# Kernel tuning notes

Measured on AMD Instinct MI355X. Metric: run time of the kernel, lower is better.

## Reference

```python
import jax, jax.numpy as jnp
import numpy as np

WS = 7          # window size
DISP = 3        # WS // 2 cyclic shift displacement
HEADS = 3
HD = 32         # head dim
DIM = 96        # hidden dim (= HEADS*HD)
DS = 4          # patch-merging downscale factor
NWH = 16        # windows per spatial dim after merging (112/7)
SCALE = HD ** -0.5


def _rel_indices(ws):
    idx = np.array([[x, y] for x in range(ws) for y in range(ws)])
    return idx[None, :, :] - idx[:, None, :] + ws - 1  # (ws^2, ws^2, 2)


def _shift_mask(ws, disp, nwh, nww):
    n = ws * ws
    ul = np.zeros((n, n), np.float32)
    ul[-disp * ws:, :-disp * ws] = -np.inf
    ul[:-disp * ws, -disp * ws:] = -np.inf
    lr = np.zeros((ws, ws, ws, ws), np.float32)
    lr[:, -disp:, :, :-disp] = -np.inf
    lr[:, :-disp, :, -disp:] = -np.inf
    lr = lr.reshape(n, n)
    m = np.zeros((nwh * nww, n, n), np.float32)
    m[-nww:] += ul            # last row of windows: upper/lower mask
    m[nww - 1::nww] += lr     # last column of windows: left/right mask
    return m

REL = jnp.asarray(_rel_indices(WS))                       # (49,49,2) int
SHIFT_MASK = jnp.asarray(_shift_mask(WS, DISP, NWH, NWH))  # (256,49,49)


def _layernorm(x, g, b):
    mu = jnp.mean(x, axis=-1, keepdims=True)
    var = jnp.var(x, axis=-1, keepdims=True)
    return (x - mu) * jax.lax.rsqrt(var + 1e-5) * g + b


def _window_attention(y, wqkv, pos_tab, wo, bo, shifted):
    # y: (b, nh, nw, DIM)
    if shifted:
        y = jnp.roll(y, (-DISP, -DISP), axis=(1, 2))
    b, nh, nw, _ = y.shape
    nwh, nww = nh // WS, nw // WS
    qkv = y @ wqkv  # (b, nh, nw, 3*DIM); last dim layout [q|k|v]
    qkv = qkv.reshape(b, nwh, WS, nww, WS, 3, HEADS, HD)
    qkv = qkv.transpose(5, 0, 6, 1, 3, 2, 4, 7).reshape(3, b, HEADS, nwh * nww, WS * WS, HD)
    q, k, v = qkv[0], qkv[1], qkv[2]
    dots = jnp.einsum('bhwid,bhwjd->bhwij', q, k) * SCALE  # (b,h,nwin,49,49)
    dots = dots + pos_tab[REL[..., 0], REL[..., 1]]        # relative pos bias
    if shifted:
        dots = dots + SHIFT_MASK[None, None]
    attn = jax.nn.softmax(dots, axis=-1)
    o = jnp.einsum('bhwij,bhwjd->bhwid', attn, v)
    o = o.reshape(b, HEADS, nwh, nww, WS, WS, HD)
    o = o.transpose(0, 2, 4, 3, 5, 1, 6).reshape(b, nh, nw, HEADS * HD)
    o = o @ wo + bo
    if shifted:
        o = jnp.roll(o, (DISP, DISP), axis=(1, 2))
    return o


def setup_inputs() -> dict:
    key = jax.random.key(0)
    ks = jax.random.split(key, 8)
    B, C, H, W = 16, 3, 448, 448
    s = 0.02
    return {
        'x': jax.random.normal(ks[0], (B, C, H, W), jnp.float32),
        'pm_w': jax.random.normal(ks[1], (C * DS * DS, DIM), jnp.float32) * s,
        'pm_b': jnp.zeros((DIM,), jnp.float32),
        'ln1_g': jnp.ones((2, DIM), jnp.float32),
        'ln1_b': jnp.zeros((2, DIM), jnp.float32),
        'qkv_w': jax.random.normal(ks[2], (2, DIM, 3 * HEADS * HD), jnp.float32) * s,
        'pos': jax.random.normal(ks[3], (2, 2 * WS - 1, 2 * WS - 1), jnp.float32),
        'out_w': jax.random.normal(ks[4], (2, HEADS * HD, DIM), jnp.float32) * s,
        'out_b': jnp.zeros((2, DIM), jnp.float32),
        'ln2_g': jnp.ones((2, DIM), jnp.float32),
        'ln2_b': jnp.zeros((2, DIM), jnp.float32),
        'ff1_w': jax.random.normal(ks[5], (2, DIM, 4 * DIM), jnp.float32) * s,
        'ff1_b': jnp.zeros((2, 4 * DIM), jnp.float32),
        'ff2_w': jax.random.normal(ks[6], (2, 4 * DIM, DIM), jnp.float32) * s,
        'ff2_b': jnp.zeros((2, DIM), jnp.float32),
    }


def reference(x, pm_w, pm_b, ln1_g, ln1_b, qkv_w, pos, out_w, out_b,
              ln2_g, ln2_b, ff1_w, ff1_b, ff2_w, ff2_b):
    b, c, h, w = x.shape
    # PatchMerging: Unfold(k=s=DS) orders channels as (c, kh, kw)
    xp = x.reshape(b, c, h // DS, DS, w // DS, DS)
    xp = xp.transpose(0, 2, 4, 1, 3, 5).reshape(b, h // DS, w // DS, c * DS * DS)
    xp = xp @ pm_w + pm_b  # (b, 112, 112, DIM)
    for i, shifted in enumerate((False, True)):
        y = _layernorm(xp, ln1_g[i], ln1_b[i])
        xp = xp + _window_attention(y, qkv_w[i], pos[i], out_w[i], out_b[i], shifted)
        y = _layernorm(xp, ln2_g[i], ln2_b[i])
        y = jax.nn.gelu(y @ ff1_w[i] + ff1_b[i], approximate=False) @ ff2_w[i] + ff2_b[i]
        xp = xp + y
    return xp.transpose(0, 3, 1, 2)  # (b, DIM, 112, 112)
```

## Files before the change

### kernel.cpp

```cpp
#include <hip/hip_runtime.h>
#include <hip/hip_bf16.h>

#define HW 112
#define NPIX (HW*HW)
#define NTOK_TOTAL (16*NPIX)
#define SCALE_ATTN 0.17677669529663689f

typedef short bf16x8 __attribute__((ext_vector_type(8)));
typedef float f32x4 __attribute__((ext_vector_type(4)));

__device__ __forceinline__ short f2bf(float f) {
    __hip_bfloat16 h = __float2bfloat16(f);
    return *reinterpret_cast<short*>(&h);
}

__device__ __forceinline__ float gelu_tanh(float x) {
    float t  = x * x;
    float m1 = fmaf(0.071354816f, t, 1.5957691f);
    float e  = __expf(x * m1);
    float r  = __builtin_amdgcn_rcpf(e + 1.0f);
    return fmaf(-x, r, x);
}

__device__ __forceinline__ void gload_lds16(const short* g, short* l) {
    __builtin_amdgcn_global_load_lds(
        (__attribute__((address_space(1))) void*)g,
        (__attribute__((address_space(3))) void*)l,
        16, 0, 0);
}

__global__ __launch_bounds__(256) void patch_merge_kernel(
    const float* __restrict__ x, const float* __restrict__ pm_w,
    const float* __restrict__ pm_b, float* __restrict__ xp)
{
    __shared__ float w_lds[48*96];
    __shared__ float in_lds[16*52];
    __shared__ float b_lds[96];
    const int t = threadIdx.x;
    const int jt = blockIdx.x, i = blockIdx.y, b = blockIdx.z;
    const int j0 = jt * 16;

    for (int e = t; e < 48*96; e += 256) w_lds[e] = pm_w[e];
    if (t < 96) b_lds[t] = pm_b[t];
    for (int e = t; e < 768; e += 256) {
        int r = e >> 6, col = e & 63;
        int c = r >> 2, kh = r & 3;
        float v = x[(((size_t)(b*3 + c))*448 + (4*i + kh))*448 + 4*j0 + col];
        in_lds[(col >> 2)*52 + c*16 + kh*4 + (col & 3)] = v;
    }
    __syncthreads();
    for (int e = t; e < 16*96; e += 256) {
        int pos = e / 96, ch = e % 96;
        float acc = b_lds[ch];
        #pragma unroll
        for (int k = 0; k < 48; ++k)
            acc = fmaf(in_lds[pos*52 + k], w_lds[k*96 + ch], acc);
        xp[((size_t)((b*HW + i)*HW) + j0 + pos)*96 + ch] = acc;
    }
}

__global__ __launch_bounds__(256) void prep_weights_kernel(
    const float* __restrict__ ff1, const float* __restrict__ ff2,
    const float* __restrict__ qkv_w, const float* __restrict__ out_w,
    const float* __restrict__ pos,
    short* __restrict__ wF, short* __restrict__ qkvT,
    short* __restrict__ outT, float* __restrict__ pos49)
{
    int i = blockIdx.x * 256 + threadIdx.x;
    if (i < 147456) {
        int l = i / 73728, r = i % 73728;
        int c = r / 18432, r2 = r % 18432;
        int half = r2 / 9216, r3 = r2 % 9216;
        int f = r3 / 512, L = (r3 % 512) / 8, j = r3 % 8;
        int ks = f / 6, n = f % 6;
        float val;
        if (half == 0) {
            int k  = ks*32 + (L >> 4)*8 + j;
            int ng = c*96 + n*16 + (L & 15);
            val = ff1[(size_t)l*36864 + (size_t)k*384 + ng];
        } else {
            int kg = c*96 + ks*32 + (L >> 4)*8 + j;
            int ng = n*16 + (L & 15);
            val = ff2[(size_t)l*36864 + (size_t)kg*96 + ng];
        }
        wF[i] = f2bf(val);
    } else if (i < 202752) {
        int j = i - 147456;
        int l = j / 27648, r = j % 27648, n = r / 96, k = r % 96;
        float v = qkv_w[(size_t)l*27648 + k*288 + n];
        if (n < 96) v *= SCALE_ATTN;
        qkvT[j] = f2bf(v);
    } else if (i < 221184) {
        int j = i - 202752;
        int l = j / 9216, r = j % 9216, n = r / 96, k = r % 96;
        outT[j] = f2bf(out_w[(size_t)l*9216 + k*96 + n]);
    } else if (i < 226280) {
        int j = i - 221184;
        int l = j / 2548, r = j % 2548, ti = r / 52, tj = r % 52;
        float v = 0.f;
        if (ti < 49 && tj < 49) {
            int xi = ti / 7, yi = ti % 7, xj = tj / 7, yj = tj % 7;
            v = pos[l*169 + (xj - xi + 6)*13 + (yj - yi + 6)];
        }
        pos49[j] = v;
    }
}

template<bool SHIFTED>
__global__ __launch_bounds__(192, 4) void attn_mfma_kernel(
    float* __restrict__ xp,
    const float* __restrict__ ln_g, const float* __restrict__ ln_b,
    const short* __restrict__ qkvT,
    const float* __restrict__ pos49,
    const short* __restrict__ outT,
    const float* __restrict__ out_b)
{
    __shared__ short bufA[6912];
    __shared__ short qk_s[13824];
    __shared__ float pos_l[2548];
    __shared__ float ob_s[96];
    __shared__ float lng[96], lnb[96];

    const int t = threadIdx.x;
    const int lane = t & 63;
    const int h = t >> 6;
    const int l15 = lane & 15, lhi = lane >> 4;
    const int wh = blockIdx.x >> 4, ww = blockIdx.x & 15;
    const int b = blockIdx.y;
    const int SH = SHIFTED ? 3 : 0;

    for (int e = t; e < 2548; e += 192) pos_l[e] = pos49[e];
    if (t < 96) { lng[t] = ln_g[t]; lnb[t] = ln_b[t]; ob_s[t] = out_b[t]; }
    __syncthreads();

    {
        const int part = t & 3;
        for (int row = t >> 2; row < 49; row += 48) {
            int ti = (row*37) >> 8, tj = row - ti*7;
            int gi = wh*7 + ti + SH; if (gi >= HW) gi -= HW;
            int gj = ww*7 + tj + SH; if (gj >= HW) gj -= HW;
            const float* src = xp + ((size_t)((b*HW + gi)*HW + gj))*96 + part*24;
            float v[24];
            #pragma unroll
            for (int q4 = 0; q4 < 6; ++q4) {
                float4 vv = *reinterpret_cast<const float4*>(src + q4*4);
                v[q4*4+0]=vv.x; v[q4*4+1]=vv.y; v[q4*4+2]=vv.z; v[q4*4+3]=vv.w;
            }
            float s = 0.f, s2 = 0.f;
            #pragma unroll
            for (int j = 0; j < 24; ++j) { s += v[j]; s2 += v[j]*v[j]; }
            s  += __shfl_xor(s, 1);  s  += __shfl_xor(s, 2);
            s2 += __shfl_xor(s2, 1); s2 += __shfl_xor(s2, 2);
            float mu = s * (1.f/96.f);
            float var = s2 * (1.f/96.f) - mu*mu;
            float rs = rsqrtf(var + 1e-5f);
            unsigned* yw = reinterpret_cast<unsigned*>(bufA) + row*52 + part*12;
            #pragma unroll
            for (int j = 0; j < 12; ++j) {
                int c = part*24 + 2*j;
                float lo = (v[2*j]   - mu)*rs*lng[c]   + lnb[c];
                float hi = (v[2*j+1] - mu)*rs*lng[c+1] + lnb[c+1];
                yw[j] = (unsigned)(unsigned short)f2bf(lo) |
                        ((unsigned)(unsigned short)f2bf(hi) << 16);
            }
        }
        for (int e = t; e < 15*52; e += 192)
            reinterpret_cast<unsigned*>(bufA)[(49 + e/52)*52 + e%52] = 0u;
    }
    __syncthreads();

    {
        f32x4 acc[2][2][4];
        #pragma unroll
        for (int p = 0; p < 2; ++p)
            #pragma unroll
            for (int s = 0; s < 2; ++s)
                #pragma unroll
                for (int m = 0; m < 4; ++m)
                    { acc[p][s][m][0]=0.f; acc[p][s][m][1]=0.f; acc[p][s][m][2]=0.f; acc[p][s][m][3]=0.f; }
        __builtin_amdgcn_s_setprio(1);
        #pragma unroll
        for (int ks = 0; ks < 3; ++ks) {
            bf16x8 a[4];
            #pragma unroll
            for (int m = 0; m < 4; ++m)
                a[m] = *reinterpret_cast<const bf16x8*>(&bufA[(m*16 + l15)*104 + ks*32 + lhi*8]);
            #pragma unroll
            for (int p = 0; p < 2; ++p)
                #pragma unroll
                for (int s = 0; s < 2; ++s) {
                    bf16x8 bf = *reinterpret_cast<const bf16x8*>(
                        qkvT + (p*96 + h*32 + s*16 + l15)*96 + ks*32 + lhi*8);
                    #pragma unroll
                    for (int m = 0; m < 4; ++m)
                        acc[p][s][m] = __builtin_amdgcn_mfma_f32_16x16x32_bf16(
                            a[m], bf, acc[p][s][m], 0, 0, 0);
                }
        }
        __builtin_amdgcn_s_setprio(0);
        #pragma unroll
        for (int p = 0; p < 2; ++p)
            #pragma unroll
            for (int s = 0; s < 2; ++s)
                #pragma unroll
                for (int m = 0; m < 4; ++m)
                    #pragma unroll
                    for (int r = 0; r < 4; ++r)
                        qk_s[h*4608 + (m*16 + lhi*4 + r)*72 + p*32 + s*16 + l15] =
                            f2bf(acc[p][s][m][r]);
    }

    float pv[4][4][4];
    {
        bf16x8 aq[4], bk[4];
        #pragma unroll
        for (int m = 0; m < 4; ++m)
            aq[m] = *reinterpret_cast<const bf16x8*>(&qk_s[h*4608 + (m*16 + l15)*72 + lhi*8]);
        #pragma unroll
        for (int n = 0; n < 4; ++n)
            bk[n] = *reinterpret_cast<const bf16x8*>(&qk_s[h*4608 + (n*16 + l15)*72 + 32 + lhi*8]);
        f32x4 sacc[4][4];
        #pragma unroll
        for (int m = 0; m < 4; ++m)
            #pragma unroll
            for (int n = 0; n < 4; ++n)
                { sacc[m][n][0]=0.f; sacc[m][n][1]=0.f; sacc[m][n][2]=0.f; sacc[m][n][3]=0.f; }
        __builtin_amdgcn_s_setprio(1);
        #pragma unroll
        for (int m = 0; m < 4; ++m)
            #pragma unroll
            for (int n = 0; n < 4; ++n)
                sacc[m][n] = __builtin_amdgcn_mfma_f32_16x16x32_bf16(aq[m], bk[n], sacc[m][n], 0, 0, 0);
        __builtin_amdgcn_s_setprio(0);

        #pragma unroll
        for (int m = 0; m < 4; ++m)
            #pragma unroll
            for (int n = 0; n < 4; ++n)
                #pragma unroll
                for (int r = 0; r < 4; ++r) {
                    int i = m*16 + lhi*4 + r, j = n*16 + l15;
                    float v;
                    if (i >= 49 || j >= 49) v = -1e30f;
                    else {
                        v = sacc[m][n][r] + pos_l[i*52 + j];
                        if (SHIFTED) {
                            if (wh == 15) {
                                int xi = (i*37) >> 8, xj = (j*37) >> 8;
                                if ((xi >= 4) != (xj >= 4)) v = -1e30f;
                            }
                            if (ww == 15) {
                                int yi = i - ((i*37) >> 8)*7, yj = j - ((j*37) >> 8)*7;
                                if ((yi >= 4) != (yj >= 4)) v = -1e30f;
                            }
                        }
                    }
                    pv[m][n][r] = v;
                }
    }
    #pragma unroll
    for (int m = 0; m < 4; ++m)
        #pragma unroll
        for (int r = 0; r < 4; ++r) {
            float mx = fmaxf(fmaxf(pv[m][0][r], pv[m][1][r]), fmaxf(pv[m][2][r], pv[m][3][r]));
            mx = fmaxf(mx, __shfl_xor(mx, 1)); mx = fmaxf(mx, __shfl_xor(mx, 2));
            mx = fmaxf(mx, __shfl_xor(mx, 4)); mx = fmaxf(mx, __shfl_xor(mx, 8));
            float e0 = __expf(pv[m][0][r] - mx), e1 = __expf(pv[m][1][r] - mx);
            float e2 = __expf(pv[m][2][r] - mx), e3 = __expf(pv[m][3][r] - mx);
            float s = e0 + e1 + e2 + e3;
            s += __shfl_xor(s, 1); s += __shfl_xor(s, 2);
            s += __shfl_xor(s, 4); s += __shfl_xor(s, 8);
            float inv = 1.f / s;
            pv[m][0][r] = e0*inv; pv[m][1][r] = e1*inv;
            pv[m][2][r] = e2*inv; pv[m][3][r] = e3*inv;
        }
    #pragma unroll
    for (int m = 0; m < 4; ++m)
        #pragma unroll
        for (int n = 0; n < 4; ++n)
            #pragma unroll
            for (int r = 0; r < 4; ++r)
                qk_s[h*4608 + (m*16 + lhi*4 + r)*72 + n*16 + l15] = f2bf(pv[m][n][r]);

    f32x4 vacc[2][4];
    #pragma unroll
    for (int s = 0; s < 2; ++s)
        #pragma unroll
        for (int m = 0; m < 4; ++m)
            { vacc[s][m][0]=0.f; vacc[s][m][1]=0.f; vacc[s][m][2]=0.f; vacc[s][m][3]=0.f; }
    __builtin_amdgcn_s_setprio(1);
    #pragma unroll
    for (int ks = 0; ks < 3; ++ks) {
        bf16x8 a[4];
        #pragma unroll
        for (int m = 0; m < 4; ++m)
            a[m] = *reinterpret_cast<const bf16x8*>(&bufA[(m*16 + l15)*104 + ks*32 + lhi*8]);
        #pragma unroll
        for (int s = 0; s < 2; ++s) {
            bf16x8 bf = *reinterpret_cast<const bf16x8*>(
                qkvT + (192 + h*32 + s*16 + l15)*96 + ks*32 + lhi*8);
            #pragma unroll
            for (int m = 0; m < 4; ++m)
                vacc[s][m] = __builtin_amdgcn_mfma_f32_16x16x32_bf16(
                    a[m], bf, vacc[s][m], 0, 0, 0);
        }
    }
    __builtin_amdgcn_s_setprio(0);
    __syncthreads();
    #pragma unroll
    for (int s = 0; s < 2; ++s)
        #pragma unroll
        for (int m = 0; m < 4; ++m)
            #pragma unroll
            for (int r = 0; r < 4; ++r)
                bufA[h*2304 + (s*16 + l15)*72 + m*16 + lhi*4 + r] = f2bf(vacc[s][m][r]);

    f32x4 oacc[2][4];
    #pragma unroll
    for (int n = 0; n < 2; ++n)
        #pragma unroll
        for (int m = 0; m < 4; ++m)
            { oacc[n][m][0]=0.f; oacc[n][m][1]=0.f; oacc[n][m][2]=0.f; oacc[n][m][3]=0.f; }
    __builtin_amdgcn_s_setprio(1);
    #pragma unroll
    for (int ks = 0; ks < 2; ++ks) {
        bf16x8 ap[4], bv[2];
        #pragma unroll
        for (int m = 0; m < 4; ++m)
            ap[m] = *reinterpret_cast<const bf16x8*>(&qk_s[h*4608 + (m*16 + l15)*72 + ks*32 + lhi*8]);
        #pragma unroll
        for (int n = 0; n < 2; ++n)
            bv[n] = *reinterpret_cast<const bf16x8*>(&bufA[h*2304 + (n*16 + l15)*72 + ks*32 + lhi*8]);
        #pragma unroll
        for (int n = 0; n < 2; ++n)
            #pragma unroll
            for (int m = 0; m < 4; ++m)
                oacc[n][m] = __builtin_amdgcn_mfma_f32_16x16x32_bf16(ap[m], bv[n], oacc[n][m], 0, 0, 0);
    }
    __builtin_amdgcn_s_setprio(0);
    __syncthreads();
    #pragma unroll
    for (int n = 0; n < 2; ++n)
        #pragma unroll
        for (int m = 0; m < 4; ++m)
            #pragma unroll
            for (int r = 0; r < 4; ++r)
                bufA[(m*16 + lhi*4 + r)*104 + h*32 + n*16 + l15] = f2bf(oacc[n][m][r]);
    __syncthreads();

    {
        f32x4 pacc[2][4];
        #pragma unroll
        for (int n = 0; n < 2; ++n)
            #pragma unroll
            for (int m = 0; m < 4; ++m)
                { pacc[n][m][0]=0.f; pacc[n][m][1]=0.f; pacc[n][m][2]=0.f; pacc[n][m][3]=0.f; }
        __builtin_amdgcn_s_setprio(1);
        #pragma unroll
        for (int ks = 0; ks < 3; ++ks) {
            bf16x8 ao[4], bw[2];
            #pragma unroll
            for (int m = 0; m < 4; ++m)
                ao[m] = *reinterpret_cast<const bf16x8*>(&bufA[(m*16 + l15)*104 + ks*32 + lhi*8]);
            #pragma unroll
            for (int n = 0; n < 2; ++n)
                bw[n] = *reinterpret_cast<const bf16x8*>(
                    outT + ((h*2 + n)*16 + l15)*96 + ks*32 + lhi*8);
            #pragma unroll
            for (int n = 0; n < 2; ++n)
                #pragma unroll
                for (int m = 0; m < 4; ++m)
                    pacc[n][m] = __builtin_amdgcn_mfma_f32_16x16x32_bf16(ao[m], bw[n], pacc[n][m], 0, 0, 0);
        }
        __builtin_amdgcn_s_setprio(0);
        #pragma unroll
        for (int m = 0; m < 4; ++m)
            #pragma unroll
            for (int r = 0; r < 4; ++r) {
                int tok = m*16 + lhi*4 + r;
                if (tok < 49) {
                    int ti = (tok*37) >> 8, tj = tok - ti*7;
                    int gi = wh*7 + ti + SH; if (gi >= HW) gi -= HW;
                    int gj = ww*7 + tj + SH; if (gj >= HW) gj -= HW;
                    float* dst = xp + ((size_t)((b*HW + gi)*HW + gj))*96;
                    #pragma unroll
                    for (int n = 0; n < 2; ++n) {
                        int ch = (h*2 + n)*16 + l15;
                        dst[ch] += pacc[n][m][r] + ob_s[ch];
                    }
                }
            }
    }
}

__global__ __launch_bounds__(256) void ff_mfma_kernel(
    float* __restrict__ xp,
    const float* __restrict__ ln_g, const float* __restrict__ ln_b,
    const short* __restrict__ wF,
    const float* __restrict__ b1,
    const float* __restrict__ b2)
{
    __shared__ short wbuf[18432];
    __shared__ short h_s[128*104];

    const int t = threadIdx.x;
    const int lane = t & 63;
    const int wv = t >> 6;
    const int l15 = lane & 15, lhi = (lane >> 4) & 3;
    const size_t tok0 = (size_t)blockIdx.x * 128 + wv*32;

    #pragma unroll
    for (int k = 0; k < 9; ++k) {
        int f = k*4 + wv;
        gload_lds16(wF + f*512 + lane*8, &wbuf[f*512]);
    }

    bf16x8 y[2][3];
    {
        float g[24], bb[24];
        #pragma unroll
        for (int ks = 0; ks < 3; ++ks)
            #pragma unroll
            for (int q = 0; q < 2; ++q) {
                float4 gv = *reinterpret_cast<const float4*>(ln_g + ks*32 + lhi*8 + q*4);
                float4 bv = *reinterpret_cast<const float4*>(ln_b + ks*32 + lhi*8 + q*4);
                g[ks*8+q*4+0]=gv.x; g[ks*8+q*4+1]=gv.y; g[ks*8+q*4+2]=gv.z; g[ks*8+q*4+3]=gv.w;
                bb[ks*8+q*4+0]=bv.x; bb[ks*8+q*4+1]=bv.y; bb[ks*8+q*4+2]=bv.z; bb[ks*8+q*4+3]=bv.w;
            }
        #pragma unroll
        for (int m = 0; m < 2; ++m) {
            const float* src = xp + (tok0 + m*16 + l15)*96 + lhi*8;
            float v[24];
            #pragma unroll
            for (int ks = 0; ks < 3; ++ks) {
                float4 a0 = *reinterpret_cast<const float4*>(src + ks*32);
                float4 a1 = *reinterpret_cast<const float4*>(src + ks*32 + 4);
                v[ks*8+0]=a0.x; v[ks*8+1]=a0.y; v[ks*8+2]=a0.z; v[ks*8+3]=a0.w;
                v[ks*8+4]=a1.x; v[ks*8+5]=a1.y; v[ks*8+6]=a1.z; v[ks*8+7]=a1.w;
            }
            float s = 0.f, s2 = 0.f;
            #pragma unroll
            for (int j = 0; j < 24; ++j) { s += v[j]; s2 += v[j]*v[j]; }
            s  += __shfl_xor(s, 16);  s  += __shfl_xor(s, 32);
            s2 += __shfl_xor(s2, 16); s2 += __shfl_xor(s2, 32);
            float mu = s * (1.f/96.f);
            float var = s2 * (1.f/96.f) - mu*mu;
            float rs = rsqrtf(var + 1e-5f);
            #pragma unroll
            for (int ks = 0; ks < 3; ++ks) {
                bf16x8 yy;
                #pragma unroll
                for (int j = 0; j < 8; ++j)
                    yy[j] = f2bf((v[ks*8+j] - mu)*rs*g[ks*8+j] + bb[ks*8+j]);
                y[m][ks] = yy;
            }
        }
    }

    f32x4 acc2[2][6];
    #pragma unroll
    for (int m = 0; m < 2; ++m)
        #pragma unroll
        for (int n = 0; n < 6; ++n)
            { acc2[m][n][0]=0.f; acc2[m][n][1]=0.f; acc2[m][n][2]=0.f; acc2[m][n][3]=0.f; }

    asm volatile("s_waitcnt vmcnt(0)" ::: "memory");
    __syncthreads();

    for (int c = 0; c < 4; ++c) {
        f32x4 acc1[2][6];
        #pragma unroll
        for (int m = 0; m < 2; ++m)
            #pragma unroll
            for (int n = 0; n < 6; ++n)
                { acc1[m][n][0]=0.f; acc1[m][n][1]=0.f; acc1[m][n][2]=0.f; acc1[m][n][3]=0.f; }
        #pragma unroll
        for (int ks = 0; ks < 3; ++ks)
            #pragma unroll
            for (int n = 0; n < 6; ++n) {
                bf16x8 bw = *reinterpret_cast<const bf16x8*>(
                    &wbuf[(ks*6 + n)*512 + lane*8]);
                #pragma unroll
                for (int m = 0; m < 2; ++m)
                    acc1[m][n] = __builtin_amdgcn_mfma_f32_16x16x32_bf16(
                        y[m][ks], bw, acc1[m][n], 0, 0, 0);
            }

        #pragma unroll
        for (int n = 0; n < 6; ++n) {
            float bias = b1[c*96 + n*16 + l15];
            #pragma unroll
            for (int m = 0; m < 2; ++m)
                #pragma unroll
                for (int r = 0; r < 4; ++r) {
                    float hv = gelu_tanh(acc1[m][n][r] + bias);
                    int row = wv*32 + m*16 + lhi*4 + r;
                    h_s[row*104 + n*16 + l15] = f2bf(hv);
                }
        }

        #pragma unroll
        for (int ks = 0; ks < 3; ++ks) {
            bf16x8 ah[2];
            #pragma unroll
            for (int m = 0; m < 2; ++m)
                ah[m] = *reinterpret_cast<const bf16x8*>(
                    &h_s[(wv*32 + m*16 + l15)*104 + ks*32 + lhi*8]);
            #pragma unroll
            for (int n = 0; n < 6; ++n) {
                bf16x8 bw = *reinterpret_cast<const bf16x8*>(
                    &wbuf[9216 + (ks*6 + n)*512 + lane*8]);
                #pragma unroll
                for (int m = 0; m < 2; ++m)
                    acc2[m][n] = __builtin_amdgcn_mfma_f32_16x16x32_bf16(
                        ah[m], bw, acc2[m][n], 0, 0, 0);
            }
        }

        if (c < 3) {
            __syncthreads();
            #pragma unroll
            for (int k = 0; k < 9; ++k) {
                int f = k*4 + wv;
                gload_lds16(wF + (c + 1)*18432 + f*512 + lane*8, &wbuf[f*512]);
            }
            asm volatile("s_waitcnt vmcnt(0)" ::: "memory");
            __syncthreads();
        }
    }

    float b2v[6];
    #pragma unroll
    for (int n = 0; n < 6; ++n) b2v[n] = b2[n*16 + l15];
    #pragma unroll
    for (int m = 0; m < 2; ++m)
        #pragma unroll
        for (int r = 0; r < 4; ++r) {
            float* dst = xp + (tok0 + m*16 + lhi*4 + r)*96 + l15;
            #pragma unroll
            for (int n = 0; n < 6; ++n)
                dst[n*16] += acc2[m][n][r] + b2v[n];
        }
}

__global__ __launch_bounds__(256) void out_kernel(
    const float* __restrict__ xp, float* __restrict__ out)
{
    __shared__ float tile[64*100];
    const int t = threadIdx.x;
    const int b = blockIdx.y;
    const int p0 = blockIdx.x * 64;
    for (int e = t; e < 64*24; e += 256) {
        int r = e / 24, p = e % 24;
        *reinterpret_cast<float4*>(&tile[r*100 + p*4]) =
            *reinterpret_cast<const float4*>(xp + ((size_t)b*NPIX + p0 + r)*96 + p*4);
    }
    __syncthreads();
    for (int e = t; e < 96*64; e += 256) {
        int ch = e >> 6, p = e & 63;
        out[((size_t)(b*96 + ch))*NPIX + p0 + p] = tile[p*100 + ch];
    }
}

extern "C" void kernel_launch(void* const* d_in, const int* in_sizes, int n_in,
                              void* d_out, int out_size, void* d_ws, size_t ws_size,
                              hipStream_t stream)
{
    (void)in_sizes; (void)n_in; (void)out_size; (void)ws_size;
    const float* x     = (const float*)d_in[0];
    const float* pm_w  = (const float*)d_in[1];
    const float* pm_b  = (const float*)d_in[2];
    const float* ln1_g = (const float*)d_in[3];
    const float* ln1_b = (const float*)d_in[4];
    const float* qkv_w = (const float*)d_in[5];
    const float* pos   = (const float*)d_in[6];
    const float* out_w = (const float*)d_in[7];
    const float* out_b = (const float*)d_in[8];
    const float* ln2_g = (const float*)d_in[9];
    const float* ln2_b = (const float*)d_in[10];
    const float* ff1_w = (const float*)d_in[11];
    const float* ff1_b = (const float*)d_in[12];
    const float* ff2_w = (const float*)d_in[13];
    const float* ff2_b = (const float*)d_in[14];

    float* xp     = (float*)d_ws;
    short* wF_b   = (short*)(xp + (size_t)NTOK_TOTAL * 96);
    short* qkvT_b = wF_b + 147456;
    short* outT_b = qkvT_b + 2*288*96;
    float* pos49_b = (float*)(outT_b + 2*96*96);

    prep_weights_kernel<<<884, 256, 0, stream>>>(ff1_w, ff2_w, qkv_w, out_w, pos,
                                                 wF_b, qkvT_b, outT_b, pos49_b);
    patch_merge_kernel<<<dim3(7, 112, 16), 256, 0, stream>>>(x, pm_w, pm_b, xp);

    for (int L = 0; L < 2; ++L) {
        if (L == 0)
            attn_mfma_kernel<false><<<dim3(256, 16), 192, 0, stream>>>(
                xp, ln1_g, ln1_b, qkvT_b, pos49_b, outT_b, out_b);
        else
            attn_mfma_kernel<true><<<dim3(256, 16), 192, 0, stream>>>(
                xp, ln1_g + 96, ln1_b + 96, qkvT_b + 27648, pos49_b + 2548,
                outT_b + 9216, out_b + 96);
        ff_mfma_kernel<<<1568, 256, 0, stream>>>(
            xp, ln2_g + L*96, ln2_b + L*96,
            wF_b + (size_t)L*73728, ff1_b + L*384, ff2_b + L*96);
    }
    out_kernel<<<dim3(196, 16), 256, 0, stream>>>(xp, (float*)d_out);
}
```

Baseline: 551.7 us.

## Split attention window rows across two waves per head, fuse V projection

The attention kernel now uses 384 threads, with two waves per head, each handling 32 of the 64 padded token rows. The V projection is computed alongside Q/K in the first MFMA loop and stored transposed in a new vT_s LDS buffer, so the second pass over the LN output is gone. An extra barrier is added and LDS use grows (bufA doubled, plus vT_s), which may lower blocks per CU. The aim is more wave-level parallelism per window and lower register pressure per wave.

```diff
diff --git a/kernel.cpp b/kernel.cpp
--- a/kernel.cpp
+++ b/kernel.cpp
@@ -107,7 +107,7 @@
 }
 
 template<bool SHIFTED>
-__global__ __launch_bounds__(192, 4) void attn_mfma_kernel(
+__global__ __launch_bounds__(384) void attn_mfma_kernel(
     float* __restrict__ xp,
     const float* __restrict__ ln_g, const float* __restrict__ ln_b,
     const short* __restrict__ qkvT,
@@ -115,27 +115,32 @@
     const short* __restrict__ outT,
     const float* __restrict__ out_b)
 {
-    __shared__ short bufA[6912];
+    __shared__ short bufA[13824];
     __shared__ short qk_s[13824];
+    __shared__ short vT_s[6912];
     __shared__ float pos_l[2548];
     __shared__ float ob_s[96];
     __shared__ float lng[96], lnb[96];
 
     const int t = threadIdx.x;
     const int lane = t & 63;
-    const int h = t >> 6;
+    const int w = t >> 6;
+    const int h = w >> 1;
+    const int half = w & 1;
     const int l15 = lane & 15, lhi = lane >> 4;
     const int wh = blockIdx.x >> 4, ww = blockIdx.x & 15;
     const int b = blockIdx.y;
     const int SH = SHIFTED ? 3 : 0;
-
-    for (int e = t; e < 2548; e += 192) pos_l[e] = pos49[e];
+    const int row0 = half*32;
+
+    for (int e = t; e < 2548; e += 384) pos_l[e] = pos49[e];
     if (t < 96) { lng[t] = ln_g[t]; lnb[t] = ln_b[t]; ob_s[t] = out_b[t]; }
     __syncthreads();
 
     {
         const int part = t & 3;
-        for (int row = t >> 2; row < 49; row += 48) {
+        int row = t >> 2;
+        if (row < 49) {
             int ti = (row*37) >> 8, tj = row - ti*7;
             int gi = wh*7 + ti + SH; if (gi >= HW) gi -= HW;
             int gj = ww*7 + tj + SH; if (gj >= HW) gj -= HW;
@@ -164,27 +169,34 @@
                         ((unsigned)(unsigned short)f2bf(hi) << 16);
             }
         }
-        for (int e = t; e < 15*52; e += 192)
+        for (int e = t; e < 15*52; e += 384)
             reinterpret_cast<unsigned*>(bufA)[(49 + e/52)*52 + e%52] = 0u;
     }
     __syncthreads();
 
     {
-        f32x4 acc[2][2][4];
+        f32x4 qk[2][2][2];
+        f32x4 vv[2][2];
         #pragma unroll
         for (int p = 0; p < 2; ++p)
             #pragma unroll
             for (int s = 0; s < 2; ++s)
                 #pragma unroll
-                for (int m = 0; m < 4; ++m)
-                    { acc[p][s][m][0]=0.f; acc[p][s][m][1]=0.f; acc[p][s][m][2]=0.f; acc[p][s][m][3]=0.f; }
+                for (int m = 0; m < 2; ++m)
+                    { qk[p][s][m][0]=0.f; qk[p][s][m][1]=0.f; qk[p][s][m][2]=0.f; qk[p][s][m][3]=0.f; }
+        #pragma unroll
+        for (int s = 0; s < 2; ++s)
+            #pragma unroll
+            for (int m = 0; m < 2; ++m)
+                { vv[s][m][0]=0.f; vv[s][m][1]=0.f; vv[s][m][2]=0.f; vv[s][m][3]=0.f; }
         __builtin_amdgcn_s_setprio(1);
         #pragma unroll
         for (int ks = 0; ks < 3; ++ks) {
-            bf16x8 a[4];
-            #pragma unroll
-            for (int m = 0; m < 4; ++m)
-                a[m] = *reinterpret_cast<const bf16x8*>(&bufA[(m*16 + l15)*104 + ks*32 + lhi*8]);
+            bf16x8 a[2];
+            #pragma unroll
+            for (int m = 0; m < 2; ++m)
+                a[m] = *reinterpret_cast<const bf16x8*>(
+                    &bufA[(row0 + m*16 + l15)*104 + ks*32 + lhi*8]);
             #pragma unroll
             for (int p = 0; p < 2; ++p)
                 #pragma unroll
@@ -192,10 +204,19 @@
                     bf16x8 bf = *reinterpret_cast<const bf16x8*>(
                         qkvT + (p*96 + h*32 + s*16 + l15)*96 + ks*32 + lhi*8);
                     #pragma unroll
-                    for (int m = 0; m < 4; ++m)
-                        acc[p][s][m] = __builtin_amdgcn_mfma_f32_16x16x32_bf16(
-                            a[m], bf, acc[p][s][m], 0, 0, 0);
+                    for (int m = 0; m < 2; ++m)
+                        qk[p][s][m] = __builtin_amdgcn_mfma_f32_16x16x32_bf16(
+                            a[m], bf, qk[p][s][m], 0, 0, 0);
                 }
+            #pragma unroll
+            for (int s = 0; s < 2; ++s) {
+                bf16x8 bf = *reinterpret_cast<const bf16x8*>(
+                    qkvT + (192 + h*32 + s*16 + l15)*96 + ks*32 + lhi*8);
+                #pragma unroll
+                for (int m = 0; m < 2; ++m)
+                    vv[s][m] = __builtin_amdgcn_mfma_f32_16x16x32_bf16(
+                        a[m], bf, vv[s][m], 0, 0, 0);
+            }
         }
         __builtin_amdgcn_s_setprio(0);
         #pragma unroll
@@ -203,43 +224,54 @@
             #pragma unroll
             for (int s = 0; s < 2; ++s)
                 #pragma unroll
-                for (int m = 0; m < 4; ++m)
+                for (int m = 0; m < 2; ++m)
                     #pragma unroll
                     for (int r = 0; r < 4; ++r)
-                        qk_s[h*4608 + (m*16 + lhi*4 + r)*72 + p*32 + s*16 + l15] =
-                            f2bf(acc[p][s][m][r]);
-    }
-
-    float pv[4][4][4];
+                        qk_s[h*4608 + (row0 + m*16 + lhi*4 + r)*72 + p*32 + s*16 + l15] =
+                            f2bf(qk[p][s][m][r]);
+        #pragma unroll
+        for (int s = 0; s < 2; ++s)
+            #pragma unroll
+            for (int m = 0; m < 2; ++m)
+                #pragma unroll
+                for (int r = 0; r < 4; ++r)
+                    vT_s[h*2304 + (s*16 + l15)*72 + row0 + m*16 + lhi*4 + r] =
+                        f2bf(vv[s][m][r]);
+    }
+    __syncthreads();
+
+    float pv[2][4][4];
     {
-        bf16x8 aq[4], bk[4];
-        #pragma unroll
-        for (int m = 0; m < 4; ++m)
-            aq[m] = *reinterpret_cast<const bf16x8*>(&qk_s[h*4608 + (m*16 + l15)*72 + lhi*8]);
+        bf16x8 aq[2], bk[4];
+        #pragma unroll
+        for (int m = 0; m < 2; ++m)
+            aq[m] = *reinterpret_cast<const bf16x8*>(
+                &qk_s[h*4608 + (row0 + m*16 + l15)*72 + lhi*8]);
         #pragma unroll
         for (int n = 0; n < 4; ++n)
-            bk[n] = *reinterpret_cast<const bf16x8*>(&qk_s[h*4608 + (n*16 + l15)*72 + 32 + lhi*8]);
-        f32x4 sacc[4][4];
-        #pragma unroll
-        for (int m = 0; m < 4; ++m)
+            bk[n] = *reinterpret_cast<const bf16x8*>(
+                &qk_s[h*4608 + (n*16 + l15)*72 + 32 + lhi*8]);
+        f32x4 sacc[2][4];
+        #pragma unroll
+        for (int m = 0; m < 2; ++m)
             #pragma unroll
             for (int n = 0; n < 4; ++n)
                 { sacc[m][n][0]=0.f; sacc[m][n][1]=0.f; sacc[m][n][2]=0.f; sacc[m][n][3]=0.f; }
         __builtin_amdgcn_s_setprio(1);
         #pragma unroll
-        for (int m = 0; m < 4; ++m)
+        for (int m = 0; m < 2; ++m)
             #pragma unroll
             for (int n = 0; n < 4; ++n)
                 sacc[m][n] = __builtin_amdgcn_mfma_f32_16x16x32_bf16(aq[m], bk[n], sacc[m][n], 0, 0, 0);
         __builtin_amdgcn_s_setprio(0);
 
         #pragma unroll
-        for (int m = 0; m < 4; ++m)
+        for (int m = 0; m < 2; ++m)
             #pragma unroll
             for (int n = 0; n < 4; ++n)
                 #pragma unroll
                 for (int r = 0; r < 4; ++r) {
-                    int i = m*16 + lhi*4 + r, j = n*16 + l15;
+                    int i = row0 + m*16 + lhi*4 + r, j = n*16 + l15;
                     float v;
                     if (i >= 49 || j >= 49) v = -1e30f;
                     else {
@@ -259,7 +291,7 @@
                 }
     }
     #pragma unroll
-    for (int m = 0; m < 4; ++m)
+    for (int m = 0; m < 2; ++m)
         #pragma unroll
         for (int r = 0; r < 4; ++r) {
             float mx = fmaxf(fmaxf(pv[m][0][r], pv[m][1][r]), fmaxf(pv[m][2][r], pv[m][3][r]));
@@ -275,66 +307,35 @@
             pv[m][2][r] = e2*inv; pv[m][3][r] = e3*inv;
         }
     #pragma unroll
-    for (int m = 0; m < 4; ++m)
+    for (int m = 0; m < 2; ++m)
         #pragma unroll
         for (int n = 0; n < 4; ++n)
             #pragma unroll
             for (int r = 0; r < 4; ++r)
-                qk_s[h*4608 + (m*16 + lhi*4 + r)*72 + n*16 + l15] = f2bf(pv[m][n][r]);
-
-    f32x4 vacc[2][4];
-    #pragma unroll
-    for (int s = 0; s < 2; ++s)
-        #pragma unroll
-        for (int m = 0; m < 4; ++m)
-            { vacc[s][m][0]=0.f; vacc[s][m][1]=0.f; vacc[s][m][2]=0.f; vacc[s][m][3]=0.f; }
-    __builtin_amdgcn_s_setprio(1);
-    #pragma unroll
-    for (int ks = 0; ks < 3; ++ks) {
-        bf16x8 a[4];
-        #pragma unroll
-        for (int m = 0; m < 4; ++m)
-            a[m] = *reinterpret_cast<const bf16x8*>(&bufA[(m*16 + l15)*104 + ks*32 + lhi*8]);
-        #pragma unroll
-        for (int s = 0; s < 2; ++s) {
-            bf16x8 bf = *reinterpret_cast<const bf16x8*>(
-                qkvT + (192 + h*32 + s*16 + l15)*96 + ks*32 + lhi*8);
-            #pragma unroll
-            for (int m = 0; m < 4; ++m)
-                vacc[s][m] = __builtin_amdgcn_mfma_f32_16x16x32_bf16(
-                    a[m], bf, vacc[s][m], 0, 0, 0);
-        }
-    }
-    __builtin_amdgcn_s_setprio(0);
-    __syncthreads();
-    #pragma unroll
-    for (int s = 0; s < 2; ++s)
-        #pragma unroll
-        for (int m = 0; m < 4; ++m)
-            #pragma unroll
-            for (int r = 0; r < 4; ++r)
-                bufA[h*2304 + (s*16 + l15)*72 + m*16 + lhi*4 + r] = f2bf(vacc[s][m][r]);
-
-    f32x4 oacc[2][4];
+                bufA[h*4608 + (row0 + m*16 + lhi*4 + r)*72 + n*16 + l15] = f2bf(pv[m][n][r]);
+
+    f32x4 oacc[2][2];
     #pragma unroll
     for (int n = 0; n < 2; ++n)
         #pragma unroll
-        for (int m = 0; m < 4; ++m)
+        for (int m = 0; m < 2; ++m)
             { oacc[n][m][0]=0.f; oacc[n][m][1]=0.f; oacc[n][m][2]=0.f; oacc[n][m][3]=0.f; }
     __builtin_amdgcn_s_setprio(1);
     #pragma unroll
     for (int ks = 0; ks < 2; ++ks) {
-        bf16x8 ap[4], bv[2];
-        #pragma unroll
-        for (int m = 0; m < 4; ++m)
-            ap[m] = *reinterpret_cast<const bf16x8*>(&qk_s[h*4608 + (m*16 + l15)*72 + ks*32 + lhi*8]);
+        bf16x8 ap[2], bv[2];
+        #pragma unroll
+        for (int m = 0; m < 2; ++m)
+            ap[m] = *reinterpret_cast<const bf16x8*>(
+                &bufA[h*4608 + (row0 + m*16 + l15)*72 + ks*32 + lhi*8]);
         #pragma unroll
         for (int n = 0; n < 2; ++n)
-            bv[n] = *reinterpret_cast<const bf16x8*>(&bufA[h*2304 + (n*16 + l15)*72 + ks*32 + lhi*8]);
+            bv[n] = *reinterpret_cast<const bf16x8*>(
+                &vT_s[h*2304 + (n*16 + l15)*72 + ks*32 + lhi*8]);
         #pragma unroll
         for (int n = 0; n < 2; ++n)
             #pragma unroll
-            for (int m = 0; m < 4; ++m)
+            for (int m = 0; m < 2; ++m)
                 oacc[n][m] = __builtin_amdgcn_mfma_f32_16x16x32_bf16(ap[m], bv[n], oacc[n][m], 0, 0, 0);
     }
     __builtin_amdgcn_s_setprio(0);
@@ -342,26 +343,27 @@
     #pragma unroll
     for (int n = 0; n < 2; ++n)
         #pragma unroll
-        for (int m = 0; m < 4; ++m)
+        for (int m = 0; m < 2; ++m)
             #pragma unroll
             for (int r = 0; r < 4; ++r)
-                bufA[(m*16 + lhi*4 + r)*104 + h*32 + n*16 + l15] = f2bf(oacc[n][m][r]);
+                bufA[(row0 + m*16 + lhi*4 + r)*104 + h*32 + n*16 + l15] = f2bf(oacc[n][m][r]);
     __syncthreads();
 
     {
-        f32x4 pacc[2][4];
+        f32x4 pacc[2][2];
         #pragma unroll
         for (int n = 0; n < 2; ++n)
             #pragma unroll
-            for (int m = 0; m < 4; ++m)
+            for (int m = 0; m < 2; ++m)
                 { pacc[n][m][0]=0.f; pacc[n][m][1]=0.f; pacc[n][m][2]=0.f; pacc[n][m][3]=0.f; }
         __builtin_amdgcn_s_setprio(1);
         #pragma unroll
         for (int ks = 0; ks < 3; ++ks) {
-            bf16x8 ao[4], bw[2];
-            #pragma unroll
-            for (int m = 0; m < 4; ++m)
-                ao[m] = *reinterpret_cast<const bf16x8*>(&bufA[(m*16 + l15)*104 + ks*32 + lhi*8]);
+            bf16x8 ao[2], bw[2];
+            #pragma unroll
+            for (int m = 0; m < 2; ++m)
+                ao[m] = *reinterpret_cast<const bf16x8*>(
+                    &bufA[(row0 + m*16 + l15)*104 + ks*32 + lhi*8]);
             #pragma unroll
             for (int n = 0; n < 2; ++n)
                 bw[n] = *reinterpret_cast<const bf16x8*>(
@@ -369,15 +371,15 @@
             #pragma unroll
             for (int n = 0; n < 2; ++n)
                 #pragma unroll
-                for (int m = 0; m < 4; ++m)
+                for (int m = 0; m < 2; ++m)
                     pacc[n][m] = __builtin_amdgcn_mfma_f32_16x16x32_bf16(ao[m], bw[n], pacc[n][m], 0, 0, 0);
         }
         __builtin_amdgcn_s_setprio(0);
         #pragma unroll
-        for (int m = 0; m < 4; ++m)
+        for (int m = 0; m < 2; ++m)
             #pragma unroll
             for (int r = 0; r < 4; ++r) {
-                int tok = m*16 + lhi*4 + r;
+                int tok = row0 + m*16 + lhi*4 + r;
                 if (tok < 49) {
                     int ti = (tok*37) >> 8, tj = tok - ti*7;
                     int gi = wh*7 + ti + SH; if (gi >= HW) gi -= HW;
@@ -595,10 +597,10 @@
 
     for (int L = 0; L < 2; ++L) {
         if (L == 0)
-            attn_mfma_kernel<false><<<dim3(256, 16), 192, 0, stream>>>(
+            attn_mfma_kernel<false><<<dim3(256, 16), 384, 0, stream>>>(
                 xp, ln1_g, ln1_b, qkvT_b, pos49_b, outT_b, out_b);
         else
-            attn_mfma_kernel<true><<<dim3(256, 16), 192, 0, stream>>>(
+            attn_mfma_kernel<true><<<dim3(256, 16), 384, 0, stream>>>(
                 xp, ln1_g + 96, ln1_b + 96, qkvT_b + 27648, pos49_b + 2548,
                 outT_b + 9216, out_b + 96);
         ff_mfma_kernel<<<1568, 256, 0, stream>>>(
```

Measured after the change: 638.8 us. 1.16x slower.

## Fuse V projection into QKV GEMM and stage V transposed in LDS

Applied to the files above, without the earlier changes.

Computes Q, K and V together in the first MFMA pass, writing V transposed into a new LDS buffer, instead of recomputing the V projection after softmax. This removes a second read of the layernormed input and the weight loads for V, and drops one barrier-separated stage. In exchange LDS use roughly grows by a third and the launch-bounds occupancy hint is removed, so fewer blocks may fit per CU and register pressure from the larger accumulator array rises.

```diff
diff --git a/kernel.cpp b/kernel.cpp
--- a/kernel.cpp
+++ b/kernel.cpp
@@ -107,7 +107,7 @@
 }
 
 template<bool SHIFTED>
-__global__ __launch_bounds__(192, 4) void attn_mfma_kernel(
+__global__ __launch_bounds__(192) void attn_mfma_kernel(
     float* __restrict__ xp,
     const float* __restrict__ ln_g, const float* __restrict__ ln_b,
     const short* __restrict__ qkvT,
@@ -115,8 +115,9 @@
     const short* __restrict__ outT,
     const float* __restrict__ out_b)
 {
-    __shared__ short bufA[6912];
+    __shared__ short bufA[13824];
     __shared__ short qk_s[13824];
+    __shared__ short vT_s[6912];
     __shared__ float pos_l[2548];
     __shared__ float ob_s[96];
     __shared__ float lng[96], lnb[96];
@@ -170,9 +171,9 @@
     __syncthreads();
 
     {
-        f32x4 acc[2][2][4];
-        #pragma unroll
-        for (int p = 0; p < 2; ++p)
+        f32x4 acc[3][2][4];
+        #pragma unroll
+        for (int p = 0; p < 3; ++p)
             #pragma unroll
             for (int s = 0; s < 2; ++s)
                 #pragma unroll
@@ -186,7 +187,7 @@
             for (int m = 0; m < 4; ++m)
                 a[m] = *reinterpret_cast<const bf16x8*>(&bufA[(m*16 + l15)*104 + ks*32 + lhi*8]);
             #pragma unroll
-            for (int p = 0; p < 2; ++p)
+            for (int p = 0; p < 3; ++p)
                 #pragma unroll
                 for (int s = 0; s < 2; ++s) {
                     bf16x8 bf = *reinterpret_cast<const bf16x8*>(
@@ -199,16 +200,22 @@
         }
         __builtin_amdgcn_s_setprio(0);
         #pragma unroll
-        for (int p = 0; p < 2; ++p)
+        for (int p = 0; p < 3; ++p)
             #pragma unroll
             for (int s = 0; s < 2; ++s)
                 #pragma unroll
                 for (int m = 0; m < 4; ++m)
                     #pragma unroll
-                    for (int r = 0; r < 4; ++r)
-                        qk_s[h*4608 + (m*16 + lhi*4 + r)*72 + p*32 + s*16 + l15] =
-                            f2bf(acc[p][s][m][r]);
-    }
+                    for (int r = 0; r < 4; ++r) {
+                        int tok = m*16 + lhi*4 + r;
+                        int c = s*16 + l15;
+                        short val = f2bf(acc[p][s][m][r]);
+                        if (p == 0)      qk_s[h*4608 + tok*72 + c] = val;
+                        else if (p == 1) qk_s[h*4608 + tok*72 + 32 + c] = val;
+                        else             vT_s[h*2304 + c*72 + tok] = val;
+                    }
+    }
+    __syncthreads();
 
     float pv[4][4][4];
     {
@@ -280,40 +287,7 @@
         for (int n = 0; n < 4; ++n)
             #pragma unroll
             for (int r = 0; r < 4; ++r)
-                qk_s[h*4608 + (m*16 + lhi*4 + r)*72 + n*16 + l15] = f2bf(pv[m][n][r]);
-
-    f32x4 vacc[2][4];
-    #pragma unroll
-    for (int s = 0; s < 2; ++s)
-        #pragma unroll
-        for (int m = 0; m < 4; ++m)
-            { vacc[s][m][0]=0.f; vacc[s][m][1]=0.f; vacc[s][m][2]=0.f; vacc[s][m][3]=0.f; }
-    __builtin_amdgcn_s_setprio(1);
-    #pragma unroll
-    for (int ks = 0; ks < 3; ++ks) {
-        bf16x8 a[4];
-        #pragma unroll
-        for (int m = 0; m < 4; ++m)
-            a[m] = *reinterpret_cast<const bf16x8*>(&bufA[(m*16 + l15)*104 + ks*32 + lhi*8]);
-        #pragma unroll
-        for (int s = 0; s < 2; ++s) {
-            bf16x8 bf = *reinterpret_cast<const bf16x8*>(
-                qkvT + (192 + h*32 + s*16 + l15)*96 + ks*32 + lhi*8);
-            #pragma unroll
-            for (int m = 0; m < 4; ++m)
-                vacc[s][m] = __builtin_amdgcn_mfma_f32_16x16x32_bf16(
-                    a[m], bf, vacc[s][m], 0, 0, 0);
-        }
-    }
-    __builtin_amdgcn_s_setprio(0);
-    __syncthreads();
-    #pragma unroll
-    for (int s = 0; s < 2; ++s)
-        #pragma unroll
-        for (int m = 0; m < 4; ++m)
-            #pragma unroll
-            for (int r = 0; r < 4; ++r)
-                bufA[h*2304 + (s*16 + l15)*72 + m*16 + lhi*4 + r] = f2bf(vacc[s][m][r]);
+                bufA[h*4608 + (m*16 + lhi*4 + r)*72 + n*16 + l15] = f2bf(pv[m][n][r]);
 
     f32x4 oacc[2][4];
     #pragma unroll
@@ -327,10 +301,10 @@
         bf16x8 ap[4], bv[2];
         #pragma unroll
         for (int m = 0; m < 4; ++m)
-            ap[m] = *reinterpret_cast<const bf16x8*>(&qk_s[h*4608 + (m*16 + l15)*72 + ks*32 + lhi*8]);
+            ap[m] = *reinterpret_cast<const bf16x8*>(&bufA[h*4608 + (m*16 + l15)*72 + ks*32 + lhi*8]);
         #pragma unroll
         for (int n = 0; n < 2; ++n)
-            bv[n] = *reinterpret_cast<const bf16x8*>(&bufA[h*2304 + (n*16 + l15)*72 + ks*32 + lhi*8]);
+            bv[n] = *reinterpret_cast<const bf16x8*>(&vT_s[h*2304 + (n*16 + l15)*72 + ks*32 + lhi*8]);
         #pragma unroll
         for (int n = 0; n < 2; ++n)
             #pragma unroll
```

Measured after the change: 555.9 us. Within noise of the previous version (+0.8%).
